# Kernel tuning notes

Hardware: AMD Instinct MI355X
Metric: run time of the kernel (lower is better)

## Reference

```python
import jax, jax.numpy as jnp
import numpy as np

HEADS = 8
EPS = 1e-5

def _layer_norm(x, gamma, beta):
    mu = jnp.mean(x, axis=-1, keepdims=True)
    var = jnp.var(x, axis=-1, keepdims=True)
    return (x - mu) * jax.lax.rsqrt(var + EPS) * gamma + beta

def setup_inputs() -> dict:
    key = jax.random.key(0)
    ks = jax.random.split(key, 12)
    B, N, D, H = 4, 2048, 512, 2048
    s = lambda d: 1.0 / np.sqrt(d)
    return {
        "x": jax.random.normal(ks[0], (B, N, D), jnp.float32),
        "w_qkv": jax.random.normal(ks[1], (D, 3 * D), jnp.float32) * s(D),
        "b_qkv": jnp.zeros((3 * D,), jnp.float32),
        "w_proj": jax.random.normal(ks[2], (D, D), jnp.float32) * s(D),
        "b_proj": jnp.zeros((D,), jnp.float32),
        "ln1_g": jnp.ones((D,), jnp.float32),
        "ln1_b": jnp.zeros((D,), jnp.float32),
        "w1": jax.random.normal(ks[3], (D, H), jnp.float32) * s(D),
        "b1": jnp.zeros((H,), jnp.float32),
        "w2": jax.random.normal(ks[4], (H, D), jnp.float32) * s(H),
        "b2": jnp.zeros((D,), jnp.float32),
        "ln2_g": jnp.ones((D,), jnp.float32),
        "ln2_b": jnp.zeros((D,), jnp.float32),
    }

def reference(x, w_qkv, b_qkv, w_proj, b_proj, ln1_g, ln1_b, w1, b1, w2, b2, ln2_g, ln2_b):
    B, N, D = x.shape
    hd = D // HEADS
    scaling = hd ** (-0.5)
    # fused QKV projection: [b, n, 3*D] -> u=3, h heads
    qkv = x @ w_qkv + b_qkv
    qkv = qkv.reshape(B, N, 3, HEADS, hd)            # 'b n (u h e)' with u outermost
    q, k, v = (qkv[:, :, 0], qkv[:, :, 1], qkv[:, :, 2])  # each [b, n, h, e]
    q = q.transpose(0, 2, 1, 3); k = k.transpose(0, 2, 1, 3); v = v.transpose(0, 2, 1, 3)
    sim = jnp.einsum('bhqe,bhke->bhqk', q, k)        # NO pre-softmax scaling
    sim = jax.nn.softmax(sim, axis=-1) * scaling     # scaling applied AFTER softmax
    att = jnp.einsum('bhqk,bhke->bhqe', sim, v)
    att = att.transpose(0, 2, 1, 3).reshape(B, N, D)
    att = att @ w_proj + b_proj
    x = _layer_norm(x + att, ln1_g, ln1_b)
    # MLP sublayer (exact GELU as in torch nn.GELU default)
    h = jax.nn.gelu(x @ w1 + b1, approximate=False) @ w2 + b2
    x = _layer_norm(x + h, ln2_g, ln2_b)
    return x
```

## Files before the change

kernel.cpp:

```cpp
#include <hip/hip_runtime.h>

#define HEADS 8
#define Bq 4
#define Nq 2048
#define Dq 512
#define Hq 2048

typedef __bf16 bf16;
typedef __bf16 bf16x8 __attribute__((ext_vector_type(8)));
typedef __bf16 bf16x4 __attribute__((ext_vector_type(4)));
typedef short short4v __attribute__((ext_vector_type(4)));
typedef float f32x4 __attribute__((ext_vector_type(4)));

__device__ __forceinline__ void gload16(const bf16* g, bf16* s) {
  __builtin_amdgcn_global_load_lds(
      (const __attribute__((address_space(1))) void*)g,
      (__attribute__((address_space(3))) void*)s, 16, 0, 0);
}

__device__ __forceinline__ float fexp2(float x) {
#if __has_builtin(__builtin_amdgcn_exp2f)
  return __builtin_amdgcn_exp2f(x);
#else
  return exp2f(x);
#endif
}

__device__ __forceinline__ f32x4 mfma16(bf16x4 a, bf16x4 b, f32x4 c) {
#if __has_builtin(__builtin_amdgcn_mfma_f32_16x16x16bf16_1k)
  return __builtin_amdgcn_mfma_f32_16x16x16bf16_1k(
      __builtin_bit_cast(short4v, a), __builtin_bit_cast(short4v, b), c, 0, 0, 0);
#else
  f32x4 d = c;
  asm("v_mfma_f32_16x16x16_bf16 %0, %1, %2, %0" : "+v"(d) : "v"(a), "v"(b));
  return d;
#endif
}

#define VM_BARRIER(N)                                         \
  do {                                                        \
    asm volatile("s_waitcnt vmcnt(" #N ")" ::: "memory");     \
    __builtin_amdgcn_s_barrier();                             \
    asm volatile("" ::: "memory");                            \
  } while (0)
#define END_BARRIER()                                         \
  do {                                                        \
    asm volatile("" ::: "memory");                            \
    __builtin_amdgcn_s_barrier();                             \
    asm volatile("" ::: "memory");                            \
  } while (0)

__global__ __launch_bounds__(256) void k_cvt_bf16(const float* __restrict__ in,
                                                  bf16* __restrict__ out, int n) {
  int i = (blockIdx.x * 256 + threadIdx.x) * 4;
  if (i >= n) return;
  float4 v = *(const float4*)(in + i);
  union { bf16 h[4]; ushort4 u; } r;
  r.h[0] = (bf16)v.x; r.h[1] = (bf16)v.y; r.h[2] = (bf16)v.z; r.h[3] = (bf16)v.w;
  *(ushort4*)(out + i) = r.u;
}

__global__ __launch_bounds__(256) void k_wtrans(const float* __restrict__ w_qkv,
                                                const float* __restrict__ w_proj,
                                                const float* __restrict__ w1,
                                                const float* __restrict__ w2,
                                                bf16* __restrict__ wqkvT,
                                                bf16* __restrict__ wprojT,
                                                bf16* __restrict__ w1T,
                                                bf16* __restrict__ w2T) {
  __shared__ float t[32][33];
  const int bid = blockIdx.x;
  const float* src;
  bf16* dst;
  int K, N, n0, k0;
  if (bid < 768) {
    src = w_qkv; dst = wqkvT; K = 512; N = 1536;
    n0 = (bid % 48) * 32; k0 = (bid / 48) * 32;
  } else if (bid < 1024) {
    int i = bid - 768;
    src = w_proj; dst = wprojT; K = 512; N = 512;
    n0 = (i % 16) * 32; k0 = (i / 16) * 32;
  } else if (bid < 2048) {
    int i = bid - 1024;
    src = w1; dst = w1T; K = 512; N = 2048;
    n0 = (i % 64) * 32; k0 = (i / 64) * 32;
  } else {
    int i = bid - 2048;
    src = w2; dst = w2T; K = 2048; N = 512;
    n0 = (i % 16) * 32; k0 = (i / 16) * 32;
  }
  const int tx = threadIdx.x, ty = threadIdx.y;
#pragma unroll
  for (int j = 0; j < 32; j += 8)
    t[ty + j][tx] = src[(size_t)(k0 + ty + j) * N + n0 + tx];
  __syncthreads();
#pragma unroll
  for (int j = 0; j < 32; j += 8)
    dst[(size_t)(n0 + ty + j) * K + k0 + tx] = (bf16)t[tx][ty + j];
}

template <int BM, bool GELU, bool RESID, bool STORE_BF16>
__global__ __launch_bounds__(512, 4) void k_gemm(const bf16* __restrict__ A,
                                                 const bf16* __restrict__ BT,
                                                 const float* __restrict__ bias,
                                                 const float* __restrict__ resid,
                                                 void* __restrict__ Cout,
                                                 int M, int N, int K, int GX) {
  constexpr int MI = BM / 32;
  constexpr int AROUNDS = BM / 64;
  constexpr size_t MAIN = (size_t)2 * (BM + 128) * 64 * 2;
  constexpr size_t CST = (size_t)BM * 136 * (STORE_BF16 ? 2 : 4);
  constexpr size_t SMEM = MAIN > CST ? MAIN : CST;
  __shared__ __align__(16) char smem[SMEM];
  bf16* Asb = (bf16*)smem;
  bf16* Bsb = Asb + 2 * BM * 64;

  const int nwg = gridDim.x;
  const int id = blockIdx.x;
  const int swz = (id & 7) * (nwg >> 3) + (id >> 3);
  const int bx = swz % GX, by = swz / GX;
  const int m0 = by * BM, n0 = bx * 128;

  const int tid = threadIdx.x, lane = tid & 63, wid = tid >> 6;
  const int wr = wid >> 2, wc = wid & 3;
  const int r16 = lane & 15, g = lane >> 4;
  const int lrow = lane >> 3;
  const int sch = (lane & 7) ^ lrow;

  f32x4 acc[MI][2] = {};

  const int NT = K >> 6;
  auto stage = [&](int t, int buf) {
    const int k0 = t << 6;
#pragma unroll
    for (int i = 0; i < AROUNDS; i++) {
      int row = i * 64 + wid * 8 + lrow;
      gload16(A + (size_t)(m0 + row) * K + k0 + sch * 8,
              Asb + buf * BM * 64 + (i * 64 + wid * 8) * 64);
    }
#pragma unroll
    for (int i = 0; i < 2; i++) {
      int row = i * 64 + wid * 8 + lrow;
      gload16(BT + (size_t)(n0 + row) * K + k0 + sch * 8,
              Bsb + buf * 128 * 64 + (i * 64 + wid * 8) * 64);
    }
  };

  stage(0, 0);
  __syncthreads();

  for (int t = 0; t < NT; t++) {
    const int cur = t & 1;
    if (t + 1 < NT) stage(t + 1, cur ^ 1);
    const bf16* Ab = Asb + cur * BM * 64;
    const bf16* Bb = Bsb + cur * 128 * 64;
#pragma unroll
    for (int kk = 0; kk < 2; kk++) {
      bf16x8 af[MI], bfr[2];
#pragma unroll
      for (int mi = 0; mi < MI; mi++)
        af[mi] = *(const bf16x8*)(Ab + (wr * (BM / 2) + mi * 16 + r16) * 64 +
                                  (((kk * 4 + g) ^ (r16 & 7)) * 8));
#pragma unroll
      for (int ni = 0; ni < 2; ni++)
        bfr[ni] = *(const bf16x8*)(Bb + (wc * 32 + ni * 16 + r16) * 64 +
                                   (((kk * 4 + g) ^ (r16 & 7)) * 8));
#pragma unroll
      for (int mi = 0; mi < MI; mi++)
#pragma unroll
        for (int ni = 0; ni < 2; ni++)
          acc[mi][ni] = __builtin_amdgcn_mfma_f32_16x16x32_bf16(af[mi], bfr[ni],
                                                                acc[mi][ni], 0, 0, 0);
    }
    __syncthreads();
  }

  float bv[2];
#pragma unroll
  for (int ni = 0; ni < 2; ni++) bv[ni] = bias[n0 + wc * 32 + ni * 16 + r16];

  if (STORE_BF16) {
    bf16* Cl = (bf16*)smem;
#pragma unroll
    for (int mi = 0; mi < MI; mi++)
#pragma unroll
      for (int ni = 0; ni < 2; ni++)
#pragma unroll
        for (int r = 0; r < 4; r++) {
          float v = acc[mi][ni][r] + bv[ni];
          if (GELU) v = 0.5f * v * (1.f + erff(v * 0.70710678118654752f));
          Cl[(wr * (BM / 2) + mi * 16 + 4 * g + r) * 136 + wc * 32 + ni * 16 + r16] =
              (bf16)v;
        }
    __syncthreads();
    constexpr int ROWS_PER = 512 * 8 / 128;
#pragma unroll
    for (int rr = 0; rr < BM / ROWS_PER; rr++) {
      int row = rr * ROWS_PER + (tid >> 4);
      int cc = (tid & 15) * 8;
      bf16x8 v = *(const bf16x8*)(Cl + row * 136 + cc);
      *(bf16x8*)((bf16*)Cout + (size_t)(m0 + row) * N + n0 + cc) = v;
    }
  } else {
    float* Cl = (float*)smem;
#pragma unroll
    for (int mi = 0; mi < MI; mi++)
#pragma unroll
      for (int ni = 0; ni < 2; ni++)
#pragma unroll
        for (int r = 0; r < 4; r++) {
          float v = acc[mi][ni][r] + bv[ni];
          if (GELU) v = 0.5f * v * (1.f + erff(v * 0.70710678118654752f));
          Cl[(wr * (BM / 2) + mi * 16 + 4 * g + r) * 136 + wc * 32 + ni * 16 + r16] = v;
        }
    __syncthreads();
    constexpr int ROWS_PER = 512 * 4 / 128;
#pragma unroll
    for (int rr = 0; rr < BM / ROWS_PER; rr++) {
      int row = rr * ROWS_PER + (tid >> 5);
      int cc = (tid & 31) * 4;
      f32x4 v = *(const f32x4*)(Cl + row * 136 + cc);
      if (RESID) {
        f32x4 rv = *(const f32x4*)(resid + (size_t)(m0 + row) * N + n0 + cc);
        v += rv;
      }
      *(f32x4*)((float*)Cout + (size_t)(m0 + row) * N + n0 + cc) = v;
    }
  }
}

__global__ __launch_bounds__(256) void k_vtrans(const bf16* __restrict__ qkv,
                                                bf16* __restrict__ vt) {
  __shared__ bf16 T[64 * 66];
  const int kvb = blockIdx.x, bh = blockIdx.y;
  const int b = bh >> 3, h = bh & 7;
  const int tid = threadIdx.x, lane = tid & 63, w = tid >> 6;
  const bf16* src = qkv + ((size_t)b * Nq + kvb * 64) * (3 * Dq) + 2 * Dq + h * 64;
#pragma unroll
  for (int i = 0; i < 2; i++) {
    int u = tid + i * 256;
    int r = u >> 3, ch = u & 7;
    *(int4*)(&T[r * 66 + ch * 8]) = *(const int4*)(src + (size_t)r * (3 * Dq) + ch * 8);
  }
  __syncthreads();
  const int kvm = 16 * ((lane >> 2) & 3) + 4 * (lane >> 4) + (lane & 3);
  bf16* dst = vt + (size_t)bh * 64 * Nq + kvb * 64 + lane;
#pragma unroll
  for (int it = 0; it < 16; it++) {
    int e = w * 16 + it;
    dst[(size_t)e * Nq] = T[kvm * 66 + e];
  }
}

__global__ __launch_bounds__(256) void k_attn(const bf16* __restrict__ qkv,
                                              const bf16* __restrict__ vt,
                                              bf16* __restrict__ att) {
  __shared__ bf16 Ks[2][64 * 64];
  __shared__ bf16 Vs[2][64 * 64];
  const int qt = blockIdx.y, b = blockIdx.x >> 3, h = blockIdx.x & 7;
  const int tid = threadIdx.x, lane = tid & 63, wid = tid >> 6;
  const int r16 = lane & 15, g = lane >> 4;
  const size_t base = (size_t)b * Nq * (3 * Dq);
  const bf16* qp = qkv + base + h * 64;
  const bf16* kp = qkv + base + Dq + h * 64;
  const bf16* vtp = vt + (size_t)(b * HEADS + h) * 64 * Nq;
  const int q0 = qt * 64 + wid * 16;

  bf16x8 qf[2];
#pragma unroll
  for (int kk = 0; kk < 2; kk++) {
    bf16x8 q = *(const bf16x8*)(qp + (size_t)(q0 + r16) * (3 * Dq) + kk * 32 + g * 8);
#pragma unroll
    for (int j = 0; j < 8; j++) q[j] = (bf16)((float)q[j] * 1.44269504f);
    qf[kk] = q;
  }

  const int srow = lane >> 3;
  const int sch = (lane & 7) ^ srow;
  const bf16x4 ones = {(bf16)1.f, (bf16)1.f, (bf16)1.f, (bf16)1.f};

  f32x4 o[4] = {};
  f32x4 ol = {};

#pragma unroll
  for (int i = 0; i < 2; i++) {
    int br = (wid * 2 + i) * 8;
    gload16(kp + (size_t)(br + srow) * (3 * Dq) + sch * 8, &Ks[0][br * 64]);
    gload16(vtp + (size_t)(br + srow) * Nq + sch * 8, &Vs[0][br * 64]);
  }
  __syncthreads();

  const int NTILES = Nq / 64;
  auto tile = [&](int t, int c) {
    if (t + 1 < NTILES) {
      const int kv1 = (t + 1) * 64;
#pragma unroll
      for (int i = 0; i < 2; i++) {
        int br = (wid * 2 + i) * 8;
        gload16(kp + (size_t)(kv1 + br + srow) * (3 * Dq) + sch * 8,
                &Ks[c ^ 1][br * 64]);
        gload16(vtp + (size_t)(br + srow) * Nq + kv1 + sch * 8, &Vs[c ^ 1][br * 64]);
      }
      VM_BARRIER(4);
    } else {
      VM_BARRIER(0);
    }

    f32x4 s[4] = {};
#pragma unroll
    for (int kk = 0; kk < 2; kk++)
#pragma unroll
      for (int nt = 0; nt < 4; nt++) {
        const bf16x8 kf = *(const bf16x8*)(
            &Ks[c][(nt * 16 + r16) * 64 + (((4 * kk + g) ^ (r16 & 7)) * 8)]);
        s[nt] = __builtin_amdgcn_mfma_f32_16x16x32_bf16(kf, qf[kk], s[nt], 0, 0, 0);
      }

#pragma unroll
    for (int nt = 0; nt < 4; nt++)
#pragma unroll
      for (int r = 0; r < 4; r++) s[nt][r] = fexp2(s[nt][r]);

    bf16x4 pk[4];
#pragma unroll
    for (int s4 = 0; s4 < 4; s4++) {
      bf16x4 p;
#pragma unroll
      for (int j = 0; j < 4; j++) p[j] = (bf16)s[s4][j];
      pk[s4] = p;
    }

    ol = mfma16(ones, pk[0], ol);
    ol = mfma16(ones, pk[1], ol);
    ol = mfma16(ones, pk[2], ol);
    ol = mfma16(ones, pk[3], ol);

#pragma unroll
    for (int ot = 0; ot < 4; ot++) {
      const int row = ot * 16 + r16;
      const bf16x8 vf0 = *(const bf16x8*)(
          &Vs[c][row * 64 + (((2 * g + 0) ^ (r16 & 7)) * 8)]);
      const bf16x8 vf1 = *(const bf16x8*)(
          &Vs[c][row * 64 + (((2 * g + 1) ^ (r16 & 7)) * 8)]);
      const bf16x4 a0 = __builtin_shufflevector(vf0, vf0, 0, 1, 2, 3);
      const bf16x4 a1 = __builtin_shufflevector(vf0, vf0, 4, 5, 6, 7);
      const bf16x4 a2 = __builtin_shufflevector(vf1, vf1, 0, 1, 2, 3);
      const bf16x4 a3 = __builtin_shufflevector(vf1, vf1, 4, 5, 6, 7);
      o[ot] = mfma16(a0, pk[0], o[ot]);
      o[ot] = mfma16(a1, pk[1], o[ot]);
      o[ot] = mfma16(a2, pk[2], o[ot]);
      o[ot] = mfma16(a3, pk[3], o[ot]);
    }
    END_BARRIER();
  };

  for (int t = 0; t < NTILES; t += 2) {
    tile(t, 0);
    tile(t + 1, 1);
  }

  asm volatile("s_nop 7\ns_nop 7");

  const float li = 0.125f / ol[0];
  const size_t rowoff = ((size_t)b * Nq + q0 + r16) * Dq + h * 64;
#pragma unroll
  for (int ot = 0; ot < 4; ot++) {
    union { bf16 h[4]; ushort4 u; } r4;
#pragma unroll
    for (int r = 0; r < 4; r++) r4.h[r] = (bf16)(o[ot][r] * li);
    *(ushort4*)(att + rowoff + ot * 16 + 4 * g) = r4.u;
  }
}

template <bool WB>
__global__ __launch_bounds__(256) void k_ln(const float* __restrict__ in,
                                            const float* __restrict__ gamma,
                                            const float* __restrict__ beta,
                                            float* __restrict__ outf,
                                            bf16* __restrict__ outb) {
  const int row = blockIdx.x * 4 + threadIdx.y;
  const int lane = threadIdx.x;
  const float* p = in + (size_t)row * Dq + lane * 8;
  float4 a = *(const float4*)p;
  float4 c = *(const float4*)(p + 4);
  float vals[8] = {a.x, a.y, a.z, a.w, c.x, c.y, c.z, c.w};
  float s = 0.f, q = 0.f;
#pragma unroll
  for (int j = 0; j < 8; j++) { s += vals[j]; q += vals[j] * vals[j]; }
#pragma unroll
  for (int off = 1; off < 64; off <<= 1) {
    s += __shfl_xor(s, off);
    q += __shfl_xor(q, off);
  }
  float mean = s * (1.f / Dq);
  float var = q * (1.f / Dq) - mean * mean;
  float rstd = rsqrtf(var + 1e-5f);
  float of[8];
#pragma unroll
  for (int j = 0; j < 8; j++) {
    int col = lane * 8 + j;
    of[j] = (vals[j] - mean) * rstd * gamma[col] + beta[col];
  }
  float4* op = (float4*)(outf + (size_t)row * Dq + lane * 8);
  op[0] = make_float4(of[0], of[1], of[2], of[3]);
  op[1] = make_float4(of[4], of[5], of[6], of[7]);
  if (WB) {
    union { bf16 h[8]; ushort4 u[2]; } rr;
#pragma unroll
    for (int j = 0; j < 8; j++) rr.h[j] = (bf16)of[j];
    ushort4* ob = (ushort4*)(outb + (size_t)row * Dq + lane * 8);
    ob[0] = rr.u[0];
    ob[1] = rr.u[1];
  }
}

extern "C" void kernel_launch(void* const* d_in, const int* in_sizes, int n_in,
                              void* d_out, int out_size, void* d_ws, size_t ws_size,
                              hipStream_t stream) {
  const float* x      = (const float*)d_in[0];
  const float* w_qkv  = (const float*)d_in[1];
  const float* b_qkv  = (const float*)d_in[2];
  const float* w_proj = (const float*)d_in[3];
  const float* b_proj = (const float*)d_in[4];
  const float* ln1_g  = (const float*)d_in[5];
  const float* ln1_b  = (const float*)d_in[6];
  const float* w1     = (const float*)d_in[7];
  const float* b1     = (const float*)d_in[8];
  const float* w2     = (const float*)d_in[9];
  const float* b2     = (const float*)d_in[10];
  const float* ln2_g  = (const float*)d_in[11];
  const float* ln2_b  = (const float*)d_in[12];
  float* out = (float*)d_out;

  const int M = Bq * Nq;

  char* p = (char*)d_ws;
  auto alloc = [&](size_t bytes) -> void* {
    char* r = p;
    p += (bytes + 255) & ~(size_t)255;
    return (void*)r;
  };
  bf16* xb     = (bf16*)alloc((size_t)M * Dq * 2);
  bf16* qkvb   = (bf16*)alloc((size_t)M * 3 * Dq * 2);
  bf16* wqkvT  = (bf16*)alloc((size_t)3 * Dq * Dq * 2);
  bf16* wprojT = (bf16*)alloc((size_t)Dq * Dq * 2);
  bf16* w1T    = (bf16*)alloc((size_t)Hq * Dq * 2);
  bf16* w2T    = (bf16*)alloc((size_t)Dq * Hq * 2);
  float* y1    = (float*)alloc((size_t)M * Dq * 4);
  float* x1f   = (float*)alloc((size_t)M * Dq * 4);
  bf16* x1b    = (bf16*)alloc((size_t)M * Dq * 2);
  bf16* hb     = (bf16*)alloc((size_t)M * Hq * 2);
  bf16* attb   = xb;
  bf16* vtb    = hb;

  dim3 tb(32, 8);
  k_cvt_bf16<<<(M * Dq / 4 + 255) / 256, 256, 0, stream>>>(x, xb, M * Dq);
  k_wtrans<<<3072, tb, 0, stream>>>(w_qkv, w_proj, w1, w2, wqkvT, wprojT, w1T, w2T);

  k_gemm<128, false, false, true><<<768, 512, 0, stream>>>(
      xb, wqkvT, b_qkv, nullptr, qkvb, M, 3 * Dq, Dq, 12);
  k_vtrans<<<dim3(Nq / 64, Bq * HEADS), 256, 0, stream>>>(qkvb, vtb);
  k_attn<<<dim3(Bq * HEADS, Nq / 64), 256, 0, stream>>>(qkvb, vtb, attb);
  k_gemm<64, false, true, false><<<512, 512, 0, stream>>>(
      attb, wprojT, b_proj, x, y1, M, Dq, Dq, 4);
  k_ln<true><<<M / 4, dim3(64, 4), 0, stream>>>(y1, ln1_g, ln1_b, x1f, x1b);
  k_gemm<128, true, false, true><<<1024, 512, 0, stream>>>(
      x1b, w1T, b1, nullptr, hb, M, Hq, Dq, 16);
  k_gemm<64, false, true, false><<<512, 512, 0, stream>>>(
      hb, w2T, b2, x1f, y1, M, Dq, Hq, 4);
  k_ln<false><<<M / 4, dim3(64, 4), 0, stream>>>(y1, ln2_g, ln2_b, out, nullptr);
}
```

Baseline: 174.6 us.

## Use 16x16x32 MFMA for PV and rowsum with permuted K row loading

Replaces the 16x16x16 bf16 MFMAs in the P·V and row-sum steps with 16x16x32 MFMAs, halving the MFMA instruction count for that stage. To make the probability registers line up as the K=32 operand, the K tile rows are loaded in a permuted order (fsrc mapping), and the V transpose kernel drops its matching permutation. This changes the data layout contract between the vtrans and attention kernels and adds address arithmetic per load, with a risk of layout mismatch errors.

```diff
diff --git a/kernel.cpp b/kernel.cpp
--- a/kernel.cpp
+++ b/kernel.cpp
@@ -23,17 +23,6 @@
   return __builtin_amdgcn_exp2f(x);
 #else
   return exp2f(x);
-#endif
-}
-
-__device__ __forceinline__ f32x4 mfma16(bf16x4 a, bf16x4 b, f32x4 c) {
-#if __has_builtin(__builtin_amdgcn_mfma_f32_16x16x16bf16_1k)
-  return __builtin_amdgcn_mfma_f32_16x16x16bf16_1k(
-      __builtin_bit_cast(short4v, a), __builtin_bit_cast(short4v, b), c, 0, 0, 0);
-#else
-  f32x4 d = c;
-  asm("v_mfma_f32_16x16x16_bf16 %0, %1, %2, %0" : "+v"(d) : "v"(a), "v"(b));
-  return d;
 #endif
 }
 
@@ -243,12 +232,11 @@
     *(int4*)(&T[r * 66 + ch * 8]) = *(const int4*)(src + (size_t)r * (3 * Dq) + ch * 8);
   }
   __syncthreads();
-  const int kvm = 16 * ((lane >> 2) & 3) + 4 * (lane >> 4) + (lane & 3);
   bf16* dst = vt + (size_t)bh * 64 * Nq + kvb * 64 + lane;
 #pragma unroll
   for (int it = 0; it < 16; it++) {
     int e = w * 16 + it;
-    dst[(size_t)e * Nq] = T[kvm * 66 + e];
+    dst[(size_t)e * Nq] = T[lane * 66 + e];
   }
 }
 
@@ -277,7 +265,16 @@
 
   const int srow = lane >> 3;
   const int sch = (lane & 7) ^ srow;
-  const bf16x4 ones = {(bf16)1.f, (bf16)1.f, (bf16)1.f, (bf16)1.f};
+  int fsrc[2];
+#pragma unroll
+  for (int i = 0; i < 2; i++) {
+    int d = (wid * 2 + i) * 8 + srow;
+    fsrc[i] = ((d >> 5) << 5) + 8 * ((d & 15) >> 2) + 4 * ((d >> 4) & 1) + (d & 3);
+  }
+
+  bf16x8 ones8;
+#pragma unroll
+  for (int j = 0; j < 8; j++) ones8[j] = (bf16)1.f;
 
   f32x4 o[4] = {};
   f32x4 ol = {};
@@ -285,7 +282,7 @@
 #pragma unroll
   for (int i = 0; i < 2; i++) {
     int br = (wid * 2 + i) * 8;
-    gload16(kp + (size_t)(br + srow) * (3 * Dq) + sch * 8, &Ks[0][br * 64]);
+    gload16(kp + (size_t)fsrc[i] * (3 * Dq) + sch * 8, &Ks[0][br * 64]);
     gload16(vtp + (size_t)(br + srow) * Nq + sch * 8, &Vs[0][br * 64]);
   }
   __syncthreads();
@@ -297,7 +294,7 @@
 #pragma unroll
       for (int i = 0; i < 2; i++) {
         int br = (wid * 2 + i) * 8;
-        gload16(kp + (size_t)(kv1 + br + srow) * (3 * Dq) + sch * 8,
+        gload16(kp + (size_t)(kv1 + fsrc[i]) * (3 * Dq) + sch * 8,
                 &Ks[c ^ 1][br * 64]);
         gload16(vtp + (size_t)(br + srow) * Nq + kv1 + sch * 8, &Vs[c ^ 1][br * 64]);
       }
@@ -321,36 +318,29 @@
 #pragma unroll
       for (int r = 0; r < 4; r++) s[nt][r] = fexp2(s[nt][r]);
 
-    bf16x4 pk[4];
-#pragma unroll
-    for (int s4 = 0; s4 < 4; s4++) {
-      bf16x4 p;
-#pragma unroll
-      for (int j = 0; j < 4; j++) p[j] = (bf16)s[s4][j];
-      pk[s4] = p;
-    }
-
-    ol = mfma16(ones, pk[0], ol);
-    ol = mfma16(ones, pk[1], ol);
-    ol = mfma16(ones, pk[2], ol);
-    ol = mfma16(ones, pk[3], ol);
-
-#pragma unroll
-    for (int ot = 0; ot < 4; ot++) {
-      const int row = ot * 16 + r16;
-      const bf16x8 vf0 = *(const bf16x8*)(
-          &Vs[c][row * 64 + (((2 * g + 0) ^ (r16 & 7)) * 8)]);
-      const bf16x8 vf1 = *(const bf16x8*)(
-          &Vs[c][row * 64 + (((2 * g + 1) ^ (r16 & 7)) * 8)]);
-      const bf16x4 a0 = __builtin_shufflevector(vf0, vf0, 0, 1, 2, 3);
-      const bf16x4 a1 = __builtin_shufflevector(vf0, vf0, 4, 5, 6, 7);
-      const bf16x4 a2 = __builtin_shufflevector(vf1, vf1, 0, 1, 2, 3);
-      const bf16x4 a3 = __builtin_shufflevector(vf1, vf1, 4, 5, 6, 7);
-      o[ot] = mfma16(a0, pk[0], o[ot]);
-      o[ot] = mfma16(a1, pk[1], o[ot]);
-      o[ot] = mfma16(a2, pk[2], o[ot]);
-      o[ot] = mfma16(a3, pk[3], o[ot]);
-    }
+    bf16x8 pb[2];
+#pragma unroll
+    for (int kk = 0; kk < 2; kk++) {
+      bf16x8 t8;
+#pragma unroll
+      for (int r = 0; r < 4; r++) {
+        t8[r] = (bf16)s[2 * kk][r];
+        t8[4 + r] = (bf16)s[2 * kk + 1][r];
+      }
+      pb[kk] = t8;
+    }
+
+    ol = __builtin_amdgcn_mfma_f32_16x16x32_bf16(ones8, pb[0], ol, 0, 0, 0);
+    ol = __builtin_amdgcn_mfma_f32_16x16x32_bf16(ones8, pb[1], ol, 0, 0, 0);
+
+#pragma unroll
+    for (int kk = 0; kk < 2; kk++)
+#pragma unroll
+      for (int ot = 0; ot < 4; ot++) {
+        const bf16x8 vf = *(const bf16x8*)(
+            &Vs[c][(ot * 16 + r16) * 64 + (((kk * 4 + g) ^ (r16 & 7)) * 8)]);
+        o[ot] = __builtin_amdgcn_mfma_f32_16x16x32_bf16(vf, pb[kk], o[ot], 0, 0, 0);
+      }
     END_BARRIER();
   };
 
```

Measured after the change: 169.0 us. 1.03x faster.
